# Optimization experiments

Measured on AMD Instinct MI355X. Metric: run time of the kernel, lower is better.

The kernel has to match this reference:

```python
import jax, jax.numpy as jnp
import numpy as np

B, T, D = 16, 1024, 1024
H, HS = 16, 64  # num_heads, attention_head_size; H*HS == D
NEG_INF = -1e9


def setup_inputs() -> dict:
    key = jax.random.key(0)
    ks = jax.random.split(key, 6)
    s = 0.02
    x = jax.random.normal(ks[0], (B, T, D), dtype=jnp.float32)
    Wq = jax.random.normal(ks[1], (D, HS), dtype=jnp.float32) * s
    Wk = jax.random.normal(ks[2], (D, HS), dtype=jnp.float32) * s
    Wv = jax.random.normal(ks[3], (D, HS), dtype=jnp.float32) * s
    Wp = jax.random.normal(ks[4], (D, D), dtype=jnp.float32) * s
    bp = jax.random.normal(ks[5], (D,), dtype=jnp.float32) * s
    return {"x": x, "Wq": Wq, "Wk": Wk, "Wv": Wv, "Wp": Wp, "bp": bp}


def reference(x, Wq, Wk, Wv, Wp, bp):
    # Single shared Head (ModuleList([Head(...)] * num_heads) shares weights).
    q = jnp.einsum('btd,dh->bth', x, Wq)  # [B,T,HS]
    k = jnp.einsum('btd,dh->bth', x, Wk)
    v = jnp.einsum('btd,dh->bth', x, Wv)
    scale = 1.0 / jnp.sqrt(jnp.float32(HS))
    scores = jnp.einsum('bth,bsh->bts', q, k) * scale  # [B,T,T]
    causal = jnp.tril(jnp.ones((T, T), dtype=bool))
    scores = jnp.where(causal[None, :, :], scores, NEG_INF)
    attn = jax.nn.softmax(scores, axis=-1)
    head_out = jnp.einsum('bts,bsh->bth', attn, v)  # [B,T,HS]
    # Concatenate H identical head outputs along feature dim -> [B,T,D]
    out = jnp.tile(head_out, (1, 1, H))
    out = jnp.einsum('btd,de->bte', out, Wp) + bp
    return out
```

## Files before the change

kernel.cpp:

```cpp
#include <hip/hip_runtime.h>
#include <hip/hip_bf16.h>
#include <cstddef>

typedef __attribute__((ext_vector_type(8))) __bf16 bf16x8;
typedef __attribute__((ext_vector_type(4))) float f32x4;
typedef unsigned long long ull_t;

static __device__ __forceinline__ unsigned short f2bf(float f) {
    __bf16 h = (__bf16)f;
    return __builtin_bit_cast(unsigned short, h);
}

__global__ void prep_weights(const float* __restrict__ Wq, const float* __restrict__ Wk,
                             const float* __restrict__ Wv, const float* __restrict__ Wp,
                             unsigned short* __restrict__ Wfrag,
                             unsigned short* __restrict__ WpFrag) {
    if (blockIdx.x < 96) {
        int gid = blockIdx.x * 256 + threadIdx.x;
        int m = gid >> 13;
        int rem = gid & 8191;
        int khi = rem >> 6;
        int lcol = rem & 63;
        const float* W = (m == 0) ? Wq : (m == 1) ? Wk : Wv;
        bf16x8 v;
#pragma unroll
        for (int j = 0; j < 8; ++j)
            v[j] = (__bf16)W[(khi * 8 + j) * 64 + lcol];
        int CB = m * 4 + (lcol >> 4);
        int S = khi >> 2;
        int lane = ((khi & 3) << 4) | (lcol & 15);
        *(bf16x8*)(Wfrag + ((size_t)(CB * 32 + S) * 512 + lane * 8)) = v;
    } else {
        int gid = (blockIdx.x - 96) * 256 + threadIdx.x;
        int h = gid >> 7;
        int cc = gid & 127;
        float s0 = 0.f, s1 = 0.f, s2 = 0.f, s3 = 0.f, s4 = 0.f, s5 = 0.f, s6 = 0.f, s7 = 0.f;
#pragma unroll
        for (int j16 = 0; j16 < 16; ++j16) {
            const float* row = Wp + (size_t)(j16 * 64 + h) * 1024 + cc * 8;
            float4 a = *(const float4*)(row);
            float4 b = *(const float4*)(row + 4);
            s0 += a.x; s1 += a.y; s2 += a.z; s3 += a.w;
            s4 += b.x; s5 += b.y; s6 += b.z; s7 += b.w;
        }
        float sum[8] = {s0, s1, s2, s3, s4, s5, s6, s7};
        int sp = h >> 5, hi = (h >> 3) & 3, j = h & 7;
#pragma unroll
        for (int q = 0; q < 8; ++q) {
            int col = cc * 8 + q;
            int lane = (hi << 4) | (col & 15);
            int CB = col >> 4;
            WpFrag[(size_t)(CB * 2 + sp) * 512 + lane * 8 + j] = f2bf(sum[q]);
        }
    }
}

__global__ __launch_bounds__(256) void qkv_gemm(const float* __restrict__ x,
                                                const unsigned short* __restrict__ Wfrag,
                                                unsigned short* __restrict__ qs,
                                                unsigned short* __restrict__ ks,
                                                unsigned short* __restrict__ vT) {
    __shared__ __align__(16) unsigned short xl[2][32 * 128];

    const int tid = threadIdx.x;
    const int lane = tid & 63;
    const int w = tid >> 6;
    const int g = lane >> 4, c = lane & 15;
    const int xcd8 = blockIdx.x & 7;
    const int seq = blockIdx.x >> 3;
    const int row0 = (2 * xcd8 + (seq >> 5)) * 1024 + (seq & 31) * 32;

    const int srow = tid >> 3;
    const int scolf = (tid & 7) * 16;
    const float* xsrc = x + (size_t)(row0 + srow) * 1024 + scolf;
    const int sdst0 = srow * 256 + ((scolf * 2) ^ ((srow & 7) << 4));
    const int sdst1 = srow * 256 + ((scolf * 2 + 16) ^ ((srow & 7) << 4));

    const unsigned short* wbase = Wfrag + (size_t)(w * 3) * 32 * 512 + lane * 8;

    f32x4 acc[2][3];
#pragma unroll
    for (int mr = 0; mr < 2; ++mr)
#pragma unroll
        for (int cb = 0; cb < 3; ++cb) acc[mr][cb] = (f32x4){0.f, 0.f, 0.f, 0.f};

    float4 pre0[4], pre1[4];
#pragma unroll
    for (int i = 0; i < 4; ++i) pre0[i] = *(const float4*)(xsrc + i * 4);
#pragma unroll
    for (int i = 0; i < 4; ++i) pre1[i] = *(const float4*)(xsrc + 128 + i * 4);

    bf16x8 bP[3][6];
#pragma unroll
    for (int pp = 0; pp < 2; ++pp) {
#pragma unroll
        for (int i = 0; i < 6; ++i) {
            int SB = pp * 2 + (i / 3);
            int cb = i % 3;
            bP[pp][i] = *(const bf16x8*)(wbase + ((size_t)(cb * 32 + SB) * 512));
        }
    }

    {
        bf16x8 v0, v1;
#pragma unroll
        for (int j = 0; j < 4; ++j) { v0[j] = (__bf16)pre0[0][j]; v0[4 + j] = (__bf16)pre0[1][j]; }
#pragma unroll
        for (int j = 0; j < 4; ++j) { v1[j] = (__bf16)pre0[2][j]; v1[4 + j] = (__bf16)pre0[3][j]; }
        *(bf16x8*)((char*)xl[0] + sdst0) = v0;
        *(bf16x8*)((char*)xl[0] + sdst1) = v1;
    }
    __syncthreads();

#pragma unroll
    for (int p = 0; p < 16; ++p) {
        const int t = p >> 1;
        if ((p & 1) == 0 && t + 2 < 8) {
            if ((t & 1) == 0) {
#pragma unroll
                for (int i = 0; i < 4; ++i) pre0[i] = *(const float4*)(xsrc + (t + 2) * 128 + i * 4);
            } else {
#pragma unroll
                for (int i = 0; i < 4; ++i) pre1[i] = *(const float4*)(xsrc + (t + 2) * 128 + i * 4);
            }
        }
        if (p + 2 < 16) {
#pragma unroll
            for (int i = 0; i < 6; ++i) {
                int SB = (p + 2) * 2 + (i / 3);
                int cb = i % 3;
                bP[(p + 2) % 3][i] = *(const bf16x8*)(wbase + ((size_t)(cb * 32 + SB) * 512));
            }
        }
#pragma unroll
        for (int sl = 0; sl < 2; ++sl) {
            int s = (p & 1) * 2 + sl;
            bf16x8 af[2];
#pragma unroll
            for (int mr = 0; mr < 2; ++mr)
                af[mr] = *(const bf16x8*)((char*)xl[t & 1] + (mr * 16 + c) * 256 +
                                          ((s * 64 + g * 16) ^ ((c & 7) << 4)));
#pragma unroll
            for (int cb = 0; cb < 3; ++cb) {
                acc[0][cb] = __builtin_amdgcn_mfma_f32_16x16x32_bf16(af[0], bP[p % 3][sl * 3 + cb], acc[0][cb], 0, 0, 0);
                acc[1][cb] = __builtin_amdgcn_mfma_f32_16x16x32_bf16(af[1], bP[p % 3][sl * 3 + cb], acc[1][cb], 0, 0, 0);
            }
        }
        if (p & 1) {
            if (t < 7) {
                bf16x8 v0, v1;
                if ((t & 1) == 0) {
#pragma unroll
                    for (int j = 0; j < 4; ++j) { v0[j] = (__bf16)pre1[0][j]; v0[4 + j] = (__bf16)pre1[1][j]; }
#pragma unroll
                    for (int j = 0; j < 4; ++j) { v1[j] = (__bf16)pre1[2][j]; v1[4 + j] = (__bf16)pre1[3][j]; }
                    *(bf16x8*)((char*)xl[1] + sdst0) = v0;
                    *(bf16x8*)((char*)xl[1] + sdst1) = v1;
                } else {
#pragma unroll
                    for (int j = 0; j < 4; ++j) { v0[j] = (__bf16)pre0[0][j]; v0[4 + j] = (__bf16)pre0[1][j]; }
#pragma unroll
                    for (int j = 0; j < 4; ++j) { v1[j] = (__bf16)pre0[2][j]; v1[4 + j] = (__bf16)pre0[3][j]; }
                    *(bf16x8*)((char*)xl[0] + sdst0) = v0;
                    *(bf16x8*)((char*)xl[0] + sdst1) = v1;
                }
            }
            __syncthreads();
        }
    }

    const float QSCALE = 0.125f * 1.44269504088896340736f;
#pragma unroll
    for (int mr = 0; mr < 2; ++mr) {
#pragma unroll
        for (int cb = 0; cb < 3; ++cb) {
            int col = w * 48 + cb * 16 + c;
            int rowb = row0 + mr * 16 + g * 4;
            if (col < 64) {
#pragma unroll
                for (int r = 0; r < 4; ++r)
                    qs[(size_t)(rowb + r) * 64 + col] = f2bf(acc[mr][cb][r] * QSCALE);
            } else if (col < 128) {
#pragma unroll
                for (int r = 0; r < 4; ++r)
                    ks[(size_t)(rowb + r) * 64 + (col - 64)] = f2bf(acc[mr][cb][r]);
            } else {
                int h = col - 128;
                int bb = rowb >> 10, trow = rowb & 1023;
                ull_t dv =
                    (ull_t)f2bf(acc[mr][cb][0]) |
                    ((ull_t)f2bf(acc[mr][cb][1]) << 16) |
                    ((ull_t)f2bf(acc[mr][cb][2]) << 32) |
                    ((ull_t)f2bf(acc[mr][cb][3]) << 48);
                *(ull_t*)(vT + (size_t)bb * 65536 + (size_t)h * 1024 + trow) = dv;
            }
        }
    }
}

__global__ __launch_bounds__(256) void attn_proj(const unsigned short* __restrict__ qs,
                                                 const unsigned short* __restrict__ ks,
                                                 const unsigned short* __restrict__ vT,
                                                 const unsigned short* __restrict__ WpFrag,
                                                 const float* __restrict__ bp,
                                                 float* __restrict__ out) {
    __shared__ unsigned short Plds[4][16 * 40];
    __shared__ float oL[2][1024];
    __shared__ float pL[2][256];
    __shared__ __align__(16) unsigned short hl[2][16 * 64];

    const int tid = threadIdx.x;
    const int lane = tid & 63;
    const int wid = tid >> 6;
    const int tslot = wid >> 1;
    const int half = wid & 1;
    const int g = lane >> 4, c = lane & 15;

    const int xcd = blockIdx.x & 7;
    const int k8 = blockIdx.x >> 3;
    const int bb = 2 * xcd + tslot;
    const int qidx = 63 - k8;
    const int qr0 = qidx * 16;
    const int qend = qr0 + 16;
    const int nc = (qidx >> 1) + 1;
    const int c0 = half ? (nc >> 1) : 0;
    const int c1 = half ? nc : (nc >> 1);

    const unsigned short* qbase = qs + ((size_t)bb * 1024 + qr0 + c) * 64 + g * 8;
    bf16x8 aq0 = *(const bf16x8*)(qbase);
    bf16x8 aq1 = *(const bf16x8*)(qbase + 32);

    const unsigned short* kB = ks + (size_t)bb * 1024 * 64;
    const unsigned short* vB = vT + (size_t)bb * 64 * 1024;

    f32x4 o[4];
#pragma unroll
    for (int i = 0; i < 4; ++i) o[i] = (f32x4){0.f, 0.f, 0.f, 0.f};
    float psum[4] = {0.f, 0.f, 0.f, 0.f};
    const f32x4 zero = {0.f, 0.f, 0.f, 0.f};

    bf16x8 kc0, kc1, kc2, kc3, vc0, vc1, vc2, vc3;
    if (c0 < c1) {
        const unsigned short* kp = kB + (size_t)(c0 * 32 + c) * 64 + g * 8;
        kc0 = *(const bf16x8*)(kp);
        kc1 = *(const bf16x8*)(kp + 32);
        kc2 = *(const bf16x8*)(kp + 16 * 64);
        kc3 = *(const bf16x8*)(kp + 16 * 64 + 32);
        const unsigned short* vp = vB + (size_t)c * 1024 + c0 * 32 + g * 8;
        vc0 = *(const bf16x8*)(vp);
        vc1 = *(const bf16x8*)(vp + 16 * 1024);
        vc2 = *(const bf16x8*)(vp + 32 * 1024);
        vc3 = *(const bf16x8*)(vp + 48 * 1024);
    }

    for (int ci = c0; ci < c1; ++ci) {
        const int j0 = ci * 32;
        const bool full = (j0 + 16 < qend);
        f32x4 s0 = __builtin_amdgcn_mfma_f32_16x16x32_bf16(aq0, kc0, zero, 0, 0, 0);
        s0 = __builtin_amdgcn_mfma_f32_16x16x32_bf16(aq1, kc1, s0, 0, 0, 0);
        f32x4 s1 = zero;
        if (full) {
            s1 = __builtin_amdgcn_mfma_f32_16x16x32_bf16(aq0, kc2, zero, 0, 0, 0);
            s1 = __builtin_amdgcn_mfma_f32_16x16x32_bf16(aq1, kc3, s1, 0, 0, 0);
        }

        bf16x8 kn0, kn1, kn2, kn3, vn0, vn1, vn2, vn3;
        if (ci + 1 < c1) {
            const int jn = (ci + 1) * 32;
            const unsigned short* kp = kB + (size_t)(jn + c) * 64 + g * 8;
            kn0 = *(const bf16x8*)(kp);
            kn1 = *(const bf16x8*)(kp + 32);
            kn2 = *(const bf16x8*)(kp + 16 * 64);
            kn3 = *(const bf16x8*)(kp + 16 * 64 + 32);
            const unsigned short* vp = vB + (size_t)c * 1024 + jn + g * 8;
            vn0 = *(const bf16x8*)(vp);
            vn1 = *(const bf16x8*)(vp + 16 * 1024);
            vn2 = *(const bf16x8*)(vp + 32 * 1024);
            vn3 = *(const bf16x8*)(vp + 48 * 1024);
        }

#pragma unroll
        for (int r = 0; r < 4; ++r) {
            int t = qr0 + g * 4 + r;
            float e0 = (j0 + c > t) ? 0.f : exp2f(s0[r]);
            float e1 = (!full || j0 + 16 + c > t) ? 0.f : exp2f(s1[r]);
            psum[r] += e0 + e1;
            Plds[wid][(g * 4 + r) * 40 + c]      = f2bf(e0);
            Plds[wid][(g * 4 + r) * 40 + 16 + c] = f2bf(e1);
        }
        bf16x8 pa = *(const bf16x8*)(&Plds[wid][c * 40 + g * 8]);
        o[0] = __builtin_amdgcn_mfma_f32_16x16x32_bf16(pa, vc0, o[0], 0, 0, 0);
        o[1] = __builtin_amdgcn_mfma_f32_16x16x32_bf16(pa, vc1, o[1], 0, 0, 0);
        o[2] = __builtin_amdgcn_mfma_f32_16x16x32_bf16(pa, vc2, o[2], 0, 0, 0);
        o[3] = __builtin_amdgcn_mfma_f32_16x16x32_bf16(pa, vc3, o[3], 0, 0, 0);

        kc0 = kn0; kc1 = kn1; kc2 = kn2; kc3 = kn3;
        vc0 = vn0; vc1 = vn1; vc2 = vn2; vc3 = vn3;
    }

    if (half == 1) {
#pragma unroll
        for (int hb = 0; hb < 4; ++hb)
            *(f32x4*)&oL[tslot][(hb * 64 + lane) * 4] = o[hb];
        f32x4 pv = {psum[0], psum[1], psum[2], psum[3]};
        *(f32x4*)&pL[tslot][lane * 4] = pv;
    }
    __syncthreads();
    if (half == 0) {
        f32x4 pv = *(const f32x4*)&pL[tslot][lane * 4];
        float inv[4];
#pragma unroll
        for (int r = 0; r < 4; ++r) {
            float ps = psum[r] + pv[r];
            ps += __shfl_xor(ps, 1);
            ps += __shfl_xor(ps, 2);
            ps += __shfl_xor(ps, 4);
            ps += __shfl_xor(ps, 8);
            inv[r] = 1.f / ps;
        }
#pragma unroll
        for (int hb = 0; hb < 4; ++hb) {
            f32x4 po = *(const f32x4*)&oL[tslot][(hb * 64 + lane) * 4];
#pragma unroll
            for (int r = 0; r < 4; ++r) {
                int row = g * 4 + r;
                int colb = (hb * 16 + c) * 2;
                *(unsigned short*)((char*)hl[tslot] + row * 128 + (colb ^ ((row & 7) << 4))) =
                    f2bf((o[hb][r] + po[r]) * inv[r]);
            }
        }
    }
    __syncthreads();

    bf16x8 a0t0 = *(const bf16x8*)((char*)hl[0] + c * 128 + ((g * 16) ^ ((c & 7) << 4)));
    bf16x8 a1t0 = *(const bf16x8*)((char*)hl[0] + c * 128 + ((64 + g * 16) ^ ((c & 7) << 4)));
    bf16x8 a0t1 = *(const bf16x8*)((char*)hl[1] + c * 128 + ((g * 16) ^ ((c & 7) << 4)));
    bf16x8 a1t1 = *(const bf16x8*)((char*)hl[1] + c * 128 + ((64 + g * 16) ^ ((c & 7) << 4)));
    const int b0 = 2 * xcd;
    const int b1 = 2 * xcd + 1;
    const size_t obase0 = ((size_t)b0 * 1024 + qr0) * 1024;
    const size_t obase1 = ((size_t)b1 * 1024 + qr0) * 1024;
#pragma unroll
    for (int cb = 0; cb < 16; ++cb) {
        int CB = wid * 16 + cb;
        bf16x8 wb0 = *(const bf16x8*)(WpFrag + (size_t)(CB * 2 + 0) * 512 + lane * 8);
        bf16x8 wb1 = *(const bf16x8*)(WpFrag + (size_t)(CB * 2 + 1) * 512 + lane * 8);
        f32x4 acc0 = __builtin_amdgcn_mfma_f32_16x16x32_bf16(a0t0, wb0, zero, 0, 0, 0);
        acc0 = __builtin_amdgcn_mfma_f32_16x16x32_bf16(a1t0, wb1, acc0, 0, 0, 0);
        f32x4 acc1 = __builtin_amdgcn_mfma_f32_16x16x32_bf16(a0t1, wb0, zero, 0, 0, 0);
        acc1 = __builtin_amdgcn_mfma_f32_16x16x32_bf16(a1t1, wb1, acc1, 0, 0, 0);
        int col = CB * 16 + c;
        float bias = bp[col];
#pragma unroll
        for (int r = 0; r < 4; ++r) {
            out[obase0 + (size_t)(g * 4 + r) * 1024 + col] = acc0[r] + bias;
            out[obase1 + (size_t)(g * 4 + r) * 1024 + col] = acc1[r] + bias;
        }
    }
}

extern "C" void kernel_launch(void* const* d_in, const int* in_sizes, int n_in,
                              void* d_out, int out_size, void* d_ws, size_t ws_size,
                              hipStream_t stream) {
    (void)in_sizes; (void)n_in; (void)out_size; (void)ws_size;
    const float* x  = (const float*)d_in[0];
    const float* Wq = (const float*)d_in[1];
    const float* Wk = (const float*)d_in[2];
    const float* Wv = (const float*)d_in[3];
    const float* Wp = (const float*)d_in[4];
    const float* bp = (const float*)d_in[5];
    float* out = (float*)d_out;

    const size_t NTOK = 16 * 1024;
    unsigned short* ws = (unsigned short*)d_ws;
    unsigned short* qs     = ws;
    unsigned short* ks     = qs + NTOK * 64;
    unsigned short* vT     = ks + NTOK * 64;
    unsigned short* Wfrag  = vT + NTOK * 64;
    unsigned short* WpFrag = Wfrag + 192 * 1024;

    prep_weights<<<128, 256, 0, stream>>>(Wq, Wk, Wv, Wp, Wfrag, WpFrag);
    qkv_gemm<<<512, 256, 0, stream>>>(x, Wfrag, qs, ks, vT);
    attn_proj<<<512, 256, 0, stream>>>(qs, ks, vT, WpFrag, bp, out);
}
```

Before: 55.86 us.

## Pair heavy and light causal query tiles in 512-thread attention blocks

Doubles attn_proj block size to 512 threads and halves the grid. Each block now handles four (batch, query-tile) slots: tile 63-k and its mirror tile k for two batches, so the causal work per block is balanced. The projection epilogue reuses each Wp fragment across four tiles instead of two, which halves the Wp loads per output tile. In exchange, shared-memory use per block doubles and only 256 blocks are launched, which may reduce occupancy or leave compute units idle.

```diff
diff --git a/kernel.cpp b/kernel.cpp
--- a/kernel.cpp
+++ b/kernel.cpp
@@ -198,16 +198,16 @@
     }
 }
 
-__global__ __launch_bounds__(256) void attn_proj(const unsigned short* __restrict__ qs,
+__global__ __launch_bounds__(512) void attn_proj(const unsigned short* __restrict__ qs,
                                                  const unsigned short* __restrict__ ks,
                                                  const unsigned short* __restrict__ vT,
                                                  const unsigned short* __restrict__ WpFrag,
                                                  const float* __restrict__ bp,
                                                  float* __restrict__ out) {
-    __shared__ unsigned short Plds[4][16 * 40];
-    __shared__ float oL[2][1024];
-    __shared__ float pL[2][256];
-    __shared__ __align__(16) unsigned short hl[2][16 * 64];
+    __shared__ unsigned short Plds[8][16 * 40];
+    __shared__ float oL[4][1024];
+    __shared__ float pL[4][256];
+    __shared__ __align__(16) unsigned short hl[4][16 * 64];
 
     const int tid = threadIdx.x;
     const int lane = tid & 63;
@@ -217,9 +217,9 @@
     const int g = lane >> 4, c = lane & 15;
 
     const int xcd = blockIdx.x & 7;
-    const int k8 = blockIdx.x >> 3;
-    const int bb = 2 * xcd + tslot;
-    const int qidx = 63 - k8;
+    const int k = blockIdx.x >> 3;
+    const int bb = 2 * xcd + (tslot & 1);
+    const int qidx = (tslot >> 1) == 0 ? (63 - k) : k;
     const int qr0 = qidx * 16;
     const int qend = qr0 + 16;
     const int nc = (qidx >> 1) + 1;
@@ -332,29 +332,34 @@
     }
     __syncthreads();
 
-    bf16x8 a0t0 = *(const bf16x8*)((char*)hl[0] + c * 128 + ((g * 16) ^ ((c & 7) << 4)));
-    bf16x8 a1t0 = *(const bf16x8*)((char*)hl[0] + c * 128 + ((64 + g * 16) ^ ((c & 7) << 4)));
-    bf16x8 a0t1 = *(const bf16x8*)((char*)hl[1] + c * 128 + ((g * 16) ^ ((c & 7) << 4)));
-    bf16x8 a1t1 = *(const bf16x8*)((char*)hl[1] + c * 128 + ((64 + g * 16) ^ ((c & 7) << 4)));
-    const int b0 = 2 * xcd;
-    const int b1 = 2 * xcd + 1;
-    const size_t obase0 = ((size_t)b0 * 1024 + qr0) * 1024;
-    const size_t obase1 = ((size_t)b1 * 1024 + qr0) * 1024;
-#pragma unroll
-    for (int cb = 0; cb < 16; ++cb) {
-        int CB = wid * 16 + cb;
+    bf16x8 a0t[4], a1t[4];
+#pragma unroll
+    for (int t = 0; t < 4; ++t) {
+        a0t[t] = *(const bf16x8*)((char*)hl[t] + c * 128 + ((g * 16) ^ ((c & 7) << 4)));
+        a1t[t] = *(const bf16x8*)((char*)hl[t] + c * 128 + ((64 + g * 16) ^ ((c & 7) << 4)));
+    }
+    size_t obase[4];
+#pragma unroll
+    for (int t = 0; t < 4; ++t) {
+        int bt = 2 * xcd + (t & 1);
+        int qx = (t >> 1) == 0 ? (63 - k) : k;
+        obase[t] = ((size_t)bt * 1024 + qx * 16) * 1024;
+    }
+#pragma unroll
+    for (int cb = 0; cb < 8; ++cb) {
+        int CB = wid * 8 + cb;
         bf16x8 wb0 = *(const bf16x8*)(WpFrag + (size_t)(CB * 2 + 0) * 512 + lane * 8);
         bf16x8 wb1 = *(const bf16x8*)(WpFrag + (size_t)(CB * 2 + 1) * 512 + lane * 8);
-        f32x4 acc0 = __builtin_amdgcn_mfma_f32_16x16x32_bf16(a0t0, wb0, zero, 0, 0, 0);
-        acc0 = __builtin_amdgcn_mfma_f32_16x16x32_bf16(a1t0, wb1, acc0, 0, 0, 0);
-        f32x4 acc1 = __builtin_amdgcn_mfma_f32_16x16x32_bf16(a0t1, wb0, zero, 0, 0, 0);
-        acc1 = __builtin_amdgcn_mfma_f32_16x16x32_bf16(a1t1, wb1, acc1, 0, 0, 0);
         int col = CB * 16 + c;
         float bias = bp[col];
 #pragma unroll
-        for (int r = 0; r < 4; ++r) {
-            out[obase0 + (size_t)(g * 4 + r) * 1024 + col] = acc0[r] + bias;
-            out[obase1 + (size_t)(g * 4 + r) * 1024 + col] = acc1[r] + bias;
+        for (int t = 0; t < 4; ++t) {
+            f32x4 acc = __builtin_amdgcn_mfma_f32_16x16x32_bf16(a0t[t], wb0, zero, 0, 0, 0);
+            acc = __builtin_amdgcn_mfma_f32_16x16x32_bf16(a1t[t], wb1, acc, 0, 0, 0);
+#pragma unroll
+            for (int r = 0; r < 4; ++r) {
+                out[obase[t] + (size_t)(g * 4 + r) * 1024 + col] = acc[r] + bias;
+            }
         }
     }
 }
@@ -381,5 +386,5 @@
 
     prep_weights<<<128, 256, 0, stream>>>(Wq, Wk, Wv, Wp, Wfrag, WpFrag);
     qkv_gemm<<<512, 256, 0, stream>>>(x, Wfrag, qs, ks, vT);
-    attn_proj<<<512, 256, 0, stream>>>(qs, ks, vT, WpFrag, bp, out);
-}
+    attn_proj<<<256, 512, 0, stream>>>(qs, ks, vT, WpFrag, bp, out);
+}
```

Result: no change. 56.14 us (+0.5%).
